# Optimization experiments

Hardware: AMD Instinct MI355X
Metric: run time of the kernel (lower is better)

The kernel has to match this reference:

```python
import jax, jax.numpy as jnp
import numpy as np

MARGIN = 2.0
EPS = 1e-6  # F.pairwise_distance default: norm of (x1 - x2 + eps)

N, D = 4096, 768


def setup_inputs() -> dict:
    key = jax.random.key(0)
    k1, k2, k3 = jax.random.split(key, 3)
    image_embedding = jax.random.normal(k1, (N, D), dtype=jnp.float32)
    text_embedding = jax.random.normal(k2, (N, D), dtype=jnp.float32)
    ground_truth = jax.random.randint(k3, (N, N), 0, 2, dtype=jnp.int32)
    return {
        "image_embedding": image_embedding,
        "text_embedding": text_embedding,
        "ground_truth": ground_truth,
    }


def reference(image_embedding, text_embedding, ground_truth):
    d = image_embedding.shape[1]
    # Pairwise squared distance with pairwise_distance's +eps on the diff:
    # ||a - b + eps||^2 = ||a||^2 + ||b||^2 - 2 a.b + 2 eps (sum a - sum b) + d eps^2
    sa = jnp.sum(image_embedding * image_embedding, axis=1)   # [n]
    sb = jnp.sum(text_embedding * text_embedding, axis=1)     # [n]
    dot = image_embedding @ text_embedding.T                  # [n, n]
    ra = jnp.sum(image_embedding, axis=1)                     # [n]
    rb = jnp.sum(text_embedding, axis=1)                      # [n]
    sq = (sa[:, None] + sb[None, :] - 2.0 * dot
          + 2.0 * EPS * (ra[:, None] - rb[None, :]) + d * EPS * EPS)
    dist = jnp.sqrt(jnp.maximum(sq, 0.0))                     # [n, n]
    label = ground_truth.astype(dist.dtype)
    hinge = jnp.maximum(MARGIN - dist, 0.0)
    loss = jnp.mean((1.0 - label) * dist * dist + label * hinge * hinge)
    return loss
```

## Files before the change

kernel.cpp:

```cpp
#include <hip/hip_runtime.h>
#include <hip/hip_bf16.h>
#include <stdint.h>
#include <stddef.h>


#define NROWS 4096
#define DIM   768
#define BM    128
#define BN    128
#define BK    64
#define MARGIN 2.0f
#define EPSV   1e-6f

typedef __bf16 bf16_t;
typedef bf16_t bf16x8 __attribute__((ext_vector_type(8)));
typedef bf16_t bf16x4 __attribute__((ext_vector_type(4)));
typedef float  f32x4  __attribute__((ext_vector_type(4)));
typedef unsigned long long u64;

__global__ __launch_bounds__(256) void prologue_kernel(
    const float* __restrict__ A, const float* __restrict__ B,
    const int* __restrict__ gt,
    bf16_t* __restrict__ Ab, bf16_t* __restrict__ Bb,
    float* __restrict__ sa, float* __restrict__ sb,
    float* __restrict__ ra, float* __restrict__ rb,
    u64* __restrict__ gtp, float* __restrict__ out)
{
    const int tid  = threadIdx.x;
    const int wave = tid >> 6;
    const int lane = tid & 63;
    const int bx   = blockIdx.x;

    if (bx == 0 && tid == 0) out[0] = 0.0f;

    if (bx < 2048) {
        const int isB  = bx >= 1024;
        const int row  = (bx & 1023) * 4 + wave;
        const float* X = isB ? B : A;
        bf16_t* Xb     = isB ? Bb : Ab;
        float* sdst    = isB ? sb : sa;
        float* rdst    = isB ? rb : ra;

        const float4* xr = (const float4*)(X + (size_t)row * DIM);
        bf16x4* xb = (bf16x4*)(Xb + (size_t)row * DIM);

        float sum = 0.0f, sq = 0.0f;
        #pragma unroll
        for (int j = 0; j < 3; ++j) {
            float4 v = xr[lane + 64 * j];
            bf16x4 o;
            o[0] = (bf16_t)v.x; o[1] = (bf16_t)v.y;
            o[2] = (bf16_t)v.z; o[3] = (bf16_t)v.w;
            xb[lane + 64 * j] = o;
            sum += (v.x + v.y) + (v.z + v.w);
            sq  += v.x * v.x + v.y * v.y + v.z * v.z + v.w * v.w;
        }
        #pragma unroll
        for (int off = 32; off > 0; off >>= 1) {
            sum += __shfl_down(sum, off);
            sq  += __shfl_down(sq,  off);
        }
        if (lane == 0) { rdst[row] = sum; sdst[row] = sq; }
    } else {
        const int wid = (bx - 2048) * 4 + wave;
        const size_t base = (size_t)wid * 8;
        int v[8];
        #pragma unroll
        for (int i = 0; i < 8; ++i)
            v[i] = gt[base * 64 + (size_t)i * 64 + lane];
        u64 mine = 0;
        #pragma unroll
        for (int i = 0; i < 8; ++i) {
            const u64 m = __ballot(v[i] != 0);
            if (lane == i) mine = m;
        }
        if (lane < 8) gtp[base + lane] = mine;
    }
}

__global__ __launch_bounds__(256, 4) void loss_kernel(
    const bf16_t* __restrict__ A, const bf16_t* __restrict__ B,
    const float* __restrict__ sa, const float* __restrict__ sb,
    const float* __restrict__ ra, const float* __restrict__ rb,
    const uint2* __restrict__ gtp, float* __restrict__ out)
{
    __shared__ __align__(16) bf16_t As[BM * BK];
    __shared__ __align__(16) bf16_t Bs[BN * BK];
    __shared__ float redp[4];

    const int tid  = threadIdx.x;
    const int wave = tid >> 6;
    const int lane = tid & 63;
    const int m0 = blockIdx.y * BM;
    const int n0 = blockIdx.x * BN;

    f32x4 acc[4][4] = {};

    const int lrow = lane >> 3;
    const int gc   = (lane & 7) ^ lrow;

    const int fr = lane & 15;
    const int q  = lane >> 4;
    const int wm = (wave >> 1) * 64;
    const int wn = (wave & 1) * 64;

    for (int k0 = 0; k0 < DIM; k0 += BK) {
        __syncthreads();
        #pragma unroll
        for (int s = 0; s < 4; ++s) {
            const int rowbase = s * 32 + wave * 8;
            const int grow    = rowbase + lrow;
            const bf16_t* ga = A + (size_t)(m0 + grow) * DIM + k0 + gc * 8;
            const bf16_t* gb = B + (size_t)(n0 + grow) * DIM + k0 + gc * 8;
            __builtin_amdgcn_global_load_lds(
                (const __attribute__((address_space(1))) void*)ga,
                (__attribute__((address_space(3))) void*)(As + rowbase * BK),
                16, 0, 0);
            __builtin_amdgcn_global_load_lds(
                (const __attribute__((address_space(1))) void*)gb,
                (__attribute__((address_space(3))) void*)(Bs + rowbase * BK),
                16, 0, 0);
        }
        __syncthreads();

        #pragma unroll
        for (int kk = 0; kk < 2; ++kk) {
            bf16x8 af[4], bfr[4];
            const int c = kk * 4 + q;
            #pragma unroll
            for (int i = 0; i < 4; ++i) {
                const int pos = (c ^ (fr & 7)) * 8;
                af[i]  = *(const bf16x8*)(As + (wm + i * 16 + fr) * BK + pos);
                bfr[i] = *(const bf16x8*)(Bs + (wn + i * 16 + fr) * BK + pos);
            }
            #pragma unroll
            for (int mi = 0; mi < 4; ++mi)
                #pragma unroll
                for (int ni = 0; ni < 4; ++ni)
                    acc[mi][ni] = __builtin_amdgcn_mfma_f32_16x16x32_bf16(
                        af[mi], bfr[ni], acc[mi][ni], 0, 0, 0);
        }
    }

    const int cq = lane & 15;
    const int rq = (lane >> 4) * 4;
    const int cb = (n0 + wn) >> 6;

    float sbv[4], rbv[4];
    #pragma unroll
    for (int ni = 0; ni < 4; ++ni) {
        const int col = n0 + wn + ni * 16 + cq;
        sbv[ni] = sb[col];
        rbv[ni] = rb[col];
    }

    float local = 0.0f;
    #pragma unroll
    for (int mi = 0; mi < 4; ++mi) {
        #pragma unroll
        for (int rr = 0; rr < 4; ++rr) {
            const int row = m0 + wm + mi * 16 + rq + rr;
            const float sav = sa[row];
            const float rav = ra[row];
            const uint2 w = gtp[(size_t)row * (NROWS / 64) + cb];
            #pragma unroll
            for (int ni = 0; ni < 4; ++ni) {
                const float dot = acc[mi][ni][rr];
                float sqv = sav + sbv[ni] - 2.0f * dot
                          + (2.0f * EPSV) * (rav - rbv[ni])
                          + (float)DIM * EPSV * EPSV;
                float msq  = fmaxf(sqv, 0.0f);
                float dist = sqrtf(msq);
                float h    = fmaxf(MARGIN - dist, 0.0f);
                const unsigned wd = (ni < 2) ? w.x : w.y;
                const unsigned g  = (wd >> (cq + (ni & 1) * 16)) & 1u;
                local += g ? (h * h) : msq;
            }
        }
    }

    #pragma unroll
    for (int off = 32; off > 0; off >>= 1) local += __shfl_down(local, off);
    if (lane == 0) redp[wave] = local;
    __syncthreads();
    if (tid == 0) {
        const float s = (redp[0] + redp[1]) + (redp[2] + redp[3]);
        atomicAdd(out, s * (1.0f / (4096.0f * 4096.0f)));
    }
}

extern "C" void kernel_launch(void* const* d_in, const int* in_sizes, int n_in,
                              void* d_out, int out_size, void* d_ws, size_t ws_size,
                              hipStream_t stream)
{
    const float* A  = (const float*)d_in[0];
    const float* B  = (const float*)d_in[1];
    const int*   gt = (const int*)d_in[2];
    float* out = (float*)d_out;

    char* ws = (char*)d_ws;
    const size_t NB = (size_t)NROWS * DIM * sizeof(bf16_t);
    bf16_t* Ab = (bf16_t*)(ws);
    bf16_t* Bb = (bf16_t*)(ws + NB);
    float* sa = (float*)(ws + 2 * NB);
    float* sb = (float*)(ws + 2 * NB + 16384);
    float* ra = (float*)(ws + 2 * NB + 32768);
    float* rb = (float*)(ws + 2 * NB + 49152);
    u64* gtp  = (u64*)(ws + 2 * NB + 65536);

    prologue_kernel<<<dim3(10240), 256, 0, stream>>>(
        A, B, gt, Ab, Bb, sa, sb, ra, rb, gtp, out);
    loss_kernel<<<dim3(NROWS / BN, NROWS / BM), 256, 0, stream>>>(
        Ab, Bb, sa, sb, ra, rb, (const uint2*)gtp, out);
}
```

Baseline: 147.9 us.

## Double-buffer LDS tiles, remap blocks per XCD, and skip sqrt in epilogue

Switches the GEMM main loop to BK=32 with two LDS buffers, so the next tile's global-to-LDS load overlaps the current MFMA work. A single barrier per iteration replaces two. Blocks are remapped from a 1D grid so that each XCD handles a contiguous band of rows, improving L2 reuse. The epilogue computes the loss algebraically as the sum of d2 minus the label-weighted sum. It only falls back to the sqrt and hinge path when some squared distance is below margin^2, which risks warp divergence if that happens often.

```diff
diff --git a/kernel.cpp b/kernel.cpp
--- a/kernel.cpp
+++ b/kernel.cpp
@@ -8,7 +8,8 @@
 #define DIM   768
 #define BM    128
 #define BN    128
-#define BK    64
+#define BK    32
+#define KITERS (DIM / BK)
 #define MARGIN 2.0f
 #define EPSV   1e-6f
 
@@ -84,103 +85,134 @@
     const float* __restrict__ ra, const float* __restrict__ rb,
     const uint2* __restrict__ gtp, float* __restrict__ out)
 {
-    __shared__ __align__(16) bf16_t As[BM * BK];
-    __shared__ __align__(16) bf16_t Bs[BN * BK];
-    __shared__ float redp[4];
+    __shared__ __align__(16) bf16_t As[2][BM * BK];
+    __shared__ __align__(16) bf16_t Bs[2][BN * BK];
 
     const int tid  = threadIdx.x;
     const int wave = tid >> 6;
     const int lane = tid & 63;
-    const int m0 = blockIdx.y * BM;
-    const int n0 = blockIdx.x * BN;
+
+    const int b    = blockIdx.x;
+    const int xcd  = b & 7;
+    const int slot = b >> 3;
+    const int m0 = (xcd * 4 + (slot >> 5)) * BM;
+    const int n0 = (slot & 31) * BN;
 
     f32x4 acc[4][4] = {};
-
-    const int lrow = lane >> 3;
-    const int gc   = (lane & 7) ^ lrow;
 
     const int fr = lane & 15;
     const int q  = lane >> 4;
     const int wm = (wave >> 1) * 64;
     const int wn = (wave & 1) * 64;
-
-    for (int k0 = 0; k0 < DIM; k0 += BK) {
-        __syncthreads();
-        #pragma unroll
-        for (int s = 0; s < 4; ++s) {
-            const int rowbase = s * 32 + wave * 8;
-            const int grow    = rowbase + lrow;
-            const bf16_t* ga = A + (size_t)(m0 + grow) * DIM + k0 + gc * 8;
-            const bf16_t* gb = B + (size_t)(n0 + grow) * DIM + k0 + gc * 8;
+    const int pos = (q ^ (fr & 3)) * 8;
+
+    const int lrow0 = lane >> 2;
+    const int gcx   = (lane & 3) ^ (lrow0 & 3);
+
+    auto stage = [&](int k0, int buf) {
+        #pragma unroll
+        for (int i = 0; i < 2; ++i) {
+            const int c0   = wave * 64 + i * 256;
+            const int row  = (c0 >> 2) + lrow0;
+            const bf16_t* ga = A + (size_t)(m0 + row) * DIM + k0 + gcx * 8;
+            const bf16_t* gb = B + (size_t)(n0 + row) * DIM + k0 + gcx * 8;
             __builtin_amdgcn_global_load_lds(
                 (const __attribute__((address_space(1))) void*)ga,
-                (__attribute__((address_space(3))) void*)(As + rowbase * BK),
+                (__attribute__((address_space(3))) void*)(&As[buf][c0 * 8]),
                 16, 0, 0);
             __builtin_amdgcn_global_load_lds(
                 (const __attribute__((address_space(1))) void*)gb,
-                (__attribute__((address_space(3))) void*)(Bs + rowbase * BK),
+                (__attribute__((address_space(3))) void*)(&Bs[buf][c0 * 8]),
                 16, 0, 0);
         }
+    };
+
+    stage(0, 0);
+    __syncthreads();
+
+    for (int k = 0; k < KITERS; ++k) {
+        const int buf = k & 1;
+        if (k + 1 < KITERS) stage((k + 1) * BK, buf ^ 1);
+
+        bf16x8 af[4], bfr[4];
+        #pragma unroll
+        for (int i = 0; i < 4; ++i) {
+            af[i]  = *(const bf16x8*)(&As[buf][(wm + i * 16 + fr) * BK + pos]);
+            bfr[i] = *(const bf16x8*)(&Bs[buf][(wn + i * 16 + fr) * BK + pos]);
+        }
+        #pragma unroll
+        for (int mi = 0; mi < 4; ++mi)
+            #pragma unroll
+            for (int ni = 0; ni < 4; ++ni)
+                acc[mi][ni] = __builtin_amdgcn_mfma_f32_16x16x32_bf16(
+                    af[mi], bfr[ni], acc[mi][ni], 0, 0, 0);
+
         __syncthreads();
-
-        #pragma unroll
-        for (int kk = 0; kk < 2; ++kk) {
-            bf16x8 af[4], bfr[4];
-            const int c = kk * 4 + q;
-            #pragma unroll
-            for (int i = 0; i < 4; ++i) {
-                const int pos = (c ^ (fr & 7)) * 8;
-                af[i]  = *(const bf16x8*)(As + (wm + i * 16 + fr) * BK + pos);
-                bfr[i] = *(const bf16x8*)(Bs + (wn + i * 16 + fr) * BK + pos);
-            }
-            #pragma unroll
-            for (int mi = 0; mi < 4; ++mi)
-                #pragma unroll
-                for (int ni = 0; ni < 4; ++ni)
-                    acc[mi][ni] = __builtin_amdgcn_mfma_f32_16x16x32_bf16(
-                        af[mi], bfr[ni], acc[mi][ni], 0, 0, 0);
-        }
     }
 
     const int cq = lane & 15;
     const int rq = (lane >> 4) * 4;
     const int cb = (n0 + wn) >> 6;
 
-    float sbv[4], rbv[4];
+    float cc[4];
     #pragma unroll
     for (int ni = 0; ni < 4; ++ni) {
         const int col = n0 + wn + ni * 16 + cq;
-        sbv[ni] = sb[col];
-        rbv[ni] = rb[col];
-    }
-
-    float local = 0.0f;
+        cc[ni] = sb[col] - 2.0f * EPSV * rb[col];
+    }
+
+    float s_all = 0.0f, s_g = 0.0f, dmin = 1e30f;
     #pragma unroll
     for (int mi = 0; mi < 4; ++mi) {
         #pragma unroll
         for (int rr = 0; rr < 4; ++rr) {
             const int row = m0 + wm + mi * 16 + rq + rr;
-            const float sav = sa[row];
-            const float rav = ra[row];
+            const float crr = sa[row] + 2.0f * EPSV * ra[row]
+                            + (float)DIM * EPSV * EPSV;
             const uint2 w = gtp[(size_t)row * (NROWS / 64) + cb];
             #pragma unroll
             for (int ni = 0; ni < 4; ++ni) {
-                const float dot = acc[mi][ni][rr];
-                float sqv = sav + sbv[ni] - 2.0f * dot
-                          + (2.0f * EPSV) * (rav - rbv[ni])
-                          + (float)DIM * EPSV * EPSV;
-                float msq  = fmaxf(sqv, 0.0f);
-                float dist = sqrtf(msq);
-                float h    = fmaxf(MARGIN - dist, 0.0f);
+                const float d2 = (crr + cc[ni]) - 2.0f * acc[mi][ni][rr];
+                s_all += d2;
+                dmin = fminf(dmin, d2);
                 const unsigned wd = (ni < 2) ? w.x : w.y;
-                const unsigned g  = (wd >> (cq + (ni & 1) * 16)) & 1u;
-                local += g ? (h * h) : msq;
+                const float gf = (float)((wd >> (cq + (ni & 1) * 16)) & 1u);
+                s_g = fmaf(gf, d2, s_g);
+            }
+        }
+    }
+    float local = s_all - s_g;
+
+    if (dmin < 4.0f) {
+        #pragma unroll
+        for (int mi = 0; mi < 4; ++mi) {
+            #pragma unroll
+            for (int rr = 0; rr < 4; ++rr) {
+                const int row = m0 + wm + mi * 16 + rq + rr;
+                const float crr = sa[row] + 2.0f * EPSV * ra[row]
+                                + (float)DIM * EPSV * EPSV;
+                const uint2 w = gtp[(size_t)row * (NROWS / 64) + cb];
+                #pragma unroll
+                for (int ni = 0; ni < 4; ++ni) {
+                    const float d2 = (crr + cc[ni]) - 2.0f * acc[mi][ni][rr];
+                    if (d2 < 4.0f) {
+                        const unsigned wd = (ni < 2) ? w.x : w.y;
+                        const float gf = (float)((wd >> (cq + (ni & 1) * 16)) & 1u);
+                        const float d2c  = fmaxf(d2, 0.0f);
+                        const float dist = sqrtf(d2c);
+                        const float h    = fmaxf(MARGIN - dist, 0.0f);
+                        local += (1.0f - gf) * d2c + gf * h * h - (d2 - gf * d2);
+                    }
+                }
             }
         }
     }
 
     #pragma unroll
     for (int off = 32; off > 0; off >>= 1) local += __shfl_down(local, off);
+
+    float* redp = (float*)&As[0][0];
+    __syncthreads();
     if (lane == 0) redp[wave] = local;
     __syncthreads();
     if (tid == 0) {
@@ -210,6 +242,6 @@
 
     prologue_kernel<<<dim3(10240), 256, 0, stream>>>(
         A, B, gt, Ab, Bb, sa, sb, ra, rb, gtp, out);
-    loss_kernel<<<dim3(NROWS / BN, NROWS / BM), 256, 0, stream>>>(
+    loss_kernel<<<dim3(1024), 256, 0, stream>>>(
         Ab, Bb, sa, sb, ra, rb, (const uint2*)gtp, out);
 }
```

Result: slower. 183.1 us (+23.8%).
